# Kernel tuning notes

Hardware: AMD Instinct MI355X
Metric: run time of the kernel (lower is better)

The kernel has to match this reference:

```python
import jax, jax.numpy as jnp
import numpy as np

DIM = 512; NHEAD = 8; DHEAD = 64; INNER = NHEAD * DHEAD
CTX = 1024; NOCT = int(np.ceil(np.log2(CTX))) + 1  # 11
B = 8; SEQ = 256; MEM = 768


def positional_encoding(ctx, num_oct):
    # matches Attention.positional_encoding on coords=arange(ctx).view(ctx,1),
    # start_octave = 1 - num_oct
    coords = jnp.arange(ctx, dtype=jnp.float32)[:, None, None]        # (ctx,1,1)
    octaves = jnp.arange(1 - num_oct, 1, dtype=jnp.float32)           # (num_oct,)
    mult = (2.0 ** octaves) * np.pi
    scaled = (coords * mult).reshape(ctx, num_oct)                    # (ctx, num_oct)
    return jnp.concatenate([jnp.sin(scaled), jnp.cos(scaled)], axis=-1)  # (ctx, 2*num_oct)


def get_shifts(mem, seq, ctx):
    coords = jnp.arange(mem + seq - 1, -1, -1) - (seq - 1)            # (mem+seq,)
    shifts = coords[None, :] + jnp.arange(seq)[:, None]               # (seq, mem+seq)
    oob = (shifts < 0) | (shifts > ctx - 1)
    bias = jnp.where(oob, -jnp.inf, 0.0).astype(jnp.float32)
    return jnp.clip(shifts, 0, ctx - 1), bias


def setup_inputs() -> dict:
    key = jax.random.key(0)
    ks = jax.random.split(key, 8)
    s = 0.02
    return {
        "x": jax.random.normal(ks[0], (B, SEQ, DIM), jnp.float32),
        "memory": jax.random.normal(ks[1], (B, MEM, DIM), jnp.float32),
        "W_qkv": jax.random.normal(ks[2], (DIM, 3 * INNER), jnp.float32) * s,
        "W_rel": jax.random.normal(ks[3], (2 * NOCT, INNER), jnp.float32) * s,
        "W_out": jax.random.normal(ks[4], (INNER, DIM), jnp.float32) * s,
        "b_out": jnp.zeros((DIM,), jnp.float32),
        "u_emb": jax.random.normal(ks[5], (DHEAD,), jnp.float32),
        "v_emb": jax.random.normal(ks[6], (DHEAD,), jnp.float32),
    }


def reference(x, memory, W_qkv, W_rel, W_out, b_out, u_emb, v_emb):
    b, seq, _ = x.shape
    mem = memory.shape[1]
    total = mem + seq
    scale = DHEAD ** -0.5

    shifts, bias = get_shifts(mem, seq, CTX)                          # (seq,total) each
    R = positional_encoding(CTX, NOCT)                                # (CTX, 2*NOCT)
    kr = (R @ W_rel)[shifts].reshape(seq, total, NHEAD, DHEAD)        # n m h d

    qkv = jnp.concatenate([memory, x], axis=1) @ W_qkv                # (b,total,3*INNER)
    q, k, v = jnp.split(qkv, 3, axis=-1)

    def heads(t):
        return t.reshape(b, total, NHEAD, DHEAD).transpose(0, 2, 1, 3)  # b h m d

    q = heads(q)[:, :, mem:]                                          # b h n d (queries only over x)
    k = heads(k)
    v = heads(v)

    term_a = jnp.einsum('bhnd,bhmd->bhnm', q, k)
    term_b = jnp.einsum('bhnd,nmhd->bhnm', q, kr)
    term_c = jnp.einsum('d,bhmd->bhm', u_emb, k)[:, :, None, :]        # broadcast over n
    term_d = jnp.einsum('d,nmhd->hnm', v_emb, kr)[None]                # broadcast over b

    dots = (term_a + term_b + term_c + term_d) * scale + bias          # banded -inf mask
    attn = jax.nn.softmax(dots, axis=-1)                               # dropout p=0 -> identity
    out = jnp.einsum('bhnm,bhmd->bnhd', attn, v).reshape(b, seq, INNER)
    return out @ W_out + b_out
```

## Files before the change

### kernel.cpp

```cpp
#include <hip/hip_runtime.h>
#include <hip/hip_bf16.h>
#include <math.h>

typedef unsigned short u16;
typedef unsigned int u32;
typedef __attribute__((ext_vector_type(8))) short short8;
typedef __attribute__((ext_vector_type(4))) float floatx4;

constexpr int kB     = 8;
constexpr int kSEQ   = 256;
constexpr int kMEM   = 768;
constexpr int kTOTAL = 1024;

__device__ __forceinline__ float bf2f(u16 u) {
  return __uint_as_float(((u32)u) << 16);
}
__device__ __forceinline__ u16 f2bf(float f) {
  __hip_bfloat16 h = __float2bfloat16(f);
  return *reinterpret_cast<u16*>(&h);
}
__device__ __forceinline__ void gload_lds16(const u16* g, u16* l) {
  __builtin_amdgcn_global_load_lds(
      (__attribute__((address_space(1))) const unsigned int*)g,
      (__attribute__((address_space(3))) unsigned int*)l, 16, 0, 0);
}

__device__ __forceinline__ void wtconv_body(
    const float* __restrict__ W, u16* __restrict__ Wt, int K, int N,
    int n0, int k0, int tid, float (*tile)[65])
{
  int r = tid >> 4, c4 = (tid & 15) * 4;
#pragma unroll
  for (int v = 0; v < 4; v++) {
    float4 w4 = *(const float4*)(W + (size_t)(k0 + v * 16 + r) * N + n0 + c4);
    tile[v * 16 + r][c4 + 0] = w4.x;
    tile[v * 16 + r][c4 + 1] = w4.y;
    tile[v * 16 + r][c4 + 2] = w4.z;
    tile[v * 16 + r][c4 + 3] = w4.w;
  }
  __syncthreads();
#pragma unroll
  for (int v = 0; v < 4; v++) {
    int rn = v * 16 + r;
    ushort4 o;
    o.x = f2bf(tile[c4 + 0][rn]);
    o.y = f2bf(tile[c4 + 1][rn]);
    o.z = f2bf(tile[c4 + 2][rn]);
    o.w = f2bf(tile[c4 + 3][rn]);
    *(ushort4*)(Wt + (size_t)(n0 + rn) * K + k0 + c4) = o;
  }
}

__global__ __launch_bounds__(256) void prep_kernel(
    const float* __restrict__ x, const float* __restrict__ memf,
    const float* __restrict__ W_qkv, const float* __restrict__ W_out,
    const float* __restrict__ W_rel, const float* __restrict__ v_emb,
    const float* __restrict__ u_emb,
    u16* __restrict__ Xb, u16* __restrict__ WqkvT, u16* __restrict__ WoutT,
    u16* __restrict__ Rrel_bf, float* __restrict__ vR)
{
  __shared__ float tile[64][65];
  __shared__ float pe[22];
  __shared__ float prod[512];
  int bid = blockIdx.x;
  int t = threadIdx.x;
  if (bid < 1024) {
    int s = bid;
    if (t < 22) {
      int o = (t < 11) ? t : (t - 11);
      float mult = ldexpf(3.14159265358979323846f, o - 10);
      float ang = (float)s * mult;
      pe[t] = (t < 11) ? sinf(ang) : cosf(ang);
    }
    __syncthreads();
#pragma unroll
    for (int c = 0; c < 2; c++) {
      int j = t + c * 256;
      float acc = 0.f;
#pragma unroll
      for (int o = 0; o < 22; ++o) acc += pe[o] * W_rel[o * 512 + j];
      u16 rbf = f2bf(acc);
      Rrel_bf[(size_t)s * 512 + j] = rbf;
      prod[j] = acc * v_emb[j & 63] - bf2f(rbf) * u_emb[j & 63];
    }
    __syncthreads();
    if (t < 8) {
      float a = 0.f;
#pragma unroll 8
      for (int d = 0; d < 64; d++) a += prod[t * 64 + d];
      vR[t * 1024 + s] = a * 0.125f;
    }
  } else if (bid < 3072) {
    int idx = (bid - 1024) * 256 + t;
    int row = idx >> 6, c8 = idx & 63;
    int b = row >> 10, pos = row & 1023;
    const float* src = (pos < kMEM)
        ? memf + (size_t)(b * kMEM + pos) * 512
        : x    + (size_t)(b * kSEQ + pos - kMEM) * 512;
    const float4* s4 = (const float4*)(src + c8 * 8);
    float4 a = s4[0], bb = s4[1];
    u16 tmp[8] = {f2bf(a.x),  f2bf(a.y),  f2bf(a.z),  f2bf(a.w),
                  f2bf(bb.x), f2bf(bb.y), f2bf(bb.z), f2bf(bb.w)};
    *(uint4*)(Xb + (size_t)row * 512 + c8 * 8) = *(uint4*)tmp;
  } else if (bid < 3264) {
    int r = bid - 3072;
    wtconv_body(W_qkv, WqkvT, 512, 1536, (r % 24) * 64, (r / 24) * 64, t, tile);
  } else {
    int r = bid - 3264;
    wtconv_body(W_out, WoutT, 512, 512, (r % 8) * 64, (r / 8) * 64, t, tile);
  }
}

__global__ __launch_bounds__(256) void gemm_bf16(
    const u16* __restrict__ A, const u16* __restrict__ Bt,
    int lda, int ldb, int ksteps,
    u16* __restrict__ Cbf, int ldc, int qscale, const float* __restrict__ uq)
{
  __shared__ u16 As[128 * 64];
  __shared__ u16 Bs[128 * 64];
  int tid = threadIdx.x;
  int id = blockIdx.y * gridDim.x + blockIdx.x;
  int gy = gridDim.y;
  int bm = (id % gy) * 128, bn = (id / gy) * 128;
  if (qscale && bn < 512 && ((bm >> 7) & 7) < 6) return;
  int ln = tid & 15, quad = (tid >> 4) & 3, w = tid >> 6;
  int moff = (w >> 1) * 64, noff = (w & 1) * 64;
  int l7 = ln & 7;
  floatx4 acc[4][4];
#pragma unroll
  for (int mi = 0; mi < 4; mi++)
#pragma unroll
    for (int ni = 0; ni < 4; ni++) acc[mi][ni] = (floatx4){0.f, 0.f, 0.f, 0.f};

  int srow[4], sgch[4];
#pragma unroll
  for (int v = 0; v < 4; v++) {
    int f = v * 256 + tid;
    srow[v] = f >> 3;
    sgch[v] = (f & 7) ^ ((f >> 3) & 7);
  }

  for (int ks = 0; ks < ksteps; ks++) {
    int k0 = ks * 64;
#pragma unroll
    for (int v = 0; v < 4; v++) {
      gload_lds16(A + (size_t)(bm + srow[v]) * lda + k0 + sgch[v] * 8,
                  &As[(v * 256 + tid) * 8]);
      gload_lds16(Bt + (size_t)(bn + srow[v]) * ldb + k0 + sgch[v] * 8,
                  &Bs[(v * 256 + tid) * 8]);
    }
    __syncthreads();
#pragma unroll
    for (int kb = 0; kb < 2; kb++) {
      short8 af[4], bfr[4];
#pragma unroll
      for (int mi = 0; mi < 4; mi++) {
        int row = moff + mi * 16 + ln;
        af[mi] = *(const short8*)&As[row * 64 + (((quad + 4 * kb) ^ l7) << 3)];
      }
#pragma unroll
      for (int ni = 0; ni < 4; ni++) {
        int row = noff + ni * 16 + ln;
        bfr[ni] = *(const short8*)&Bs[row * 64 + (((quad + 4 * kb) ^ l7) << 3)];
      }
#pragma unroll
      for (int mi = 0; mi < 4; mi++)
#pragma unroll
        for (int ni = 0; ni < 4; ni++)
          acc[mi][ni] = __builtin_amdgcn_mfma_f32_16x16x32_bf16(
              af[mi], bfr[ni], acc[mi][ni], 0, 0, 0);
    }
    __syncthreads();
  }

  int r0 = bm + moff + quad * 4;
#pragma unroll
  for (int ni = 0; ni < 4; ni++) {
    int col = bn + noff + ni * 16 + ln;
    bool isq = qscale && col < 512;
    float scale = isq ? 0.125f : 1.f;
    float uadd = isq ? uq[col & 63] : 0.f;
#pragma unroll
    for (int mi = 0; mi < 4; mi++) {
#pragma unroll
      for (int r = 0; r < 4; r++) {
        int row = r0 + mi * 16 + r;
        Cbf[(size_t)row * ldc + col] = f2bf((acc[mi][ni][r] + uadd) * scale);
      }
    }
  }
}

__global__ __launch_bounds__(256) void gemm_bf16_64(
    const u16* __restrict__ A, const u16* __restrict__ Bt,
    int lda, int ldb, int ksteps,
    float* __restrict__ Cf, int ldc, const float* __restrict__ bias)
{
  __shared__ u16 As[64 * 64];
  __shared__ u16 Bs[64 * 64];
  int tid = threadIdx.x;
  int id = blockIdx.y * gridDim.x + blockIdx.x;
  int gy = gridDim.y;
  int bm = (id % gy) * 64, bn = (id / gy) * 64;
  int ln = tid & 15, quad = (tid >> 4) & 3, w = tid >> 6;
  int moff = (w >> 1) * 32, noff = (w & 1) * 32;
  int l7 = ln & 7;
  floatx4 acc[2][2];
#pragma unroll
  for (int mi = 0; mi < 2; mi++)
#pragma unroll
    for (int ni = 0; ni < 2; ni++) acc[mi][ni] = (floatx4){0.f, 0.f, 0.f, 0.f};

  int srow[2], sgch[2];
#pragma unroll
  for (int v = 0; v < 2; v++) {
    int f = v * 256 + tid;
    srow[v] = f >> 3;
    sgch[v] = (f & 7) ^ ((f >> 3) & 7);
  }

  for (int ks = 0; ks < ksteps; ks++) {
    int k0 = ks * 64;
#pragma unroll
    for (int v = 0; v < 2; v++) {
      gload_lds16(A + (size_t)(bm + srow[v]) * lda + k0 + sgch[v] * 8,
                  &As[(v * 256 + tid) * 8]);
      gload_lds16(Bt + (size_t)(bn + srow[v]) * ldb + k0 + sgch[v] * 8,
                  &Bs[(v * 256 + tid) * 8]);
    }
    __syncthreads();
#pragma unroll
    for (int kb = 0; kb < 2; kb++) {
      short8 af[2], bfr[2];
#pragma unroll
      for (int mi = 0; mi < 2; mi++) {
        int row = moff + mi * 16 + ln;
        af[mi] = *(const short8*)&As[row * 64 + (((quad + 4 * kb) ^ l7) << 3)];
      }
#pragma unroll
      for (int ni = 0; ni < 2; ni++) {
        int row = noff + ni * 16 + ln;
        bfr[ni] = *(const short8*)&Bs[row * 64 + (((quad + 4 * kb) ^ l7) << 3)];
      }
#pragma unroll
      for (int mi = 0; mi < 2; mi++)
#pragma unroll
        for (int ni = 0; ni < 2; ni++)
          acc[mi][ni] = __builtin_amdgcn_mfma_f32_16x16x32_bf16(
              af[mi], bfr[ni], acc[mi][ni], 0, 0, 0);
    }
    __syncthreads();
  }

  int r0 = bm + moff + quad * 4;
#pragma unroll
  for (int ni = 0; ni < 2; ni++) {
    int col = bn + noff + ni * 16 + ln;
    float cv = bias[col];
#pragma unroll
    for (int mi = 0; mi < 2; mi++) {
#pragma unroll
      for (int r = 0; r < 4; r++) {
        int row = r0 + mi * 16 + r;
        Cf[(size_t)row * ldc + col] = acc[mi][ni][r] + cv;
      }
    }
  }
}

__global__ __launch_bounds__(256) void attn_mfma(
    const u16* __restrict__ qkv_bf, const u16* __restrict__ Rrel_bf,
    const float* __restrict__ vR,
    u16* __restrict__ Opart, float* __restrict__ lbuf)
{
  constexpr int LD = 72;
  __shared__ u16 Vt[4][64 * LD];
  __shared__ u16 Ps[64 * LD];

  int h = blockIdx.x;
  int nt = blockIdx.y >> 1, p = blockIdx.y & 1;
  int b = blockIdx.z;
  int n0 = nt * 64, bh = b * 8 + h;
  int tid = threadIdx.x;
  int w = tid >> 6, lane = tid & 63;
  int l15 = lane & 15, quad = lane >> 4, q8 = quad * 8;

  int sr0 = tid >> 3, sc8 = tid & 7;
  int sr1 = (256 + tid) >> 3;
  int vg0 = ((sr0 >> 3) ^ sc8) * 8 + (sr0 & 7);
  int vg1 = ((sr1 >> 3) ^ sc8) * 8 + (sr1 & 7);

  const u16* kpart = qkv_bf + (size_t)(b * kTOTAL) * 1536 + 512 + h * 64;
  const float* vRh = vR + h * 1024;
  int s_base_w = kMEM + n0 + 16 * w;

  const u16* qrow = qkv_bf + (size_t)(b * kTOTAL + kMEM + n0 + 16 * w + l15) * 1536 + h * 64;
  short8 qf0 = *(const short8*)(qrow + q8);
  short8 qf1 = *(const short8*)(qrow + 32 + q8);

  int bidx[4];
#pragma unroll
  for (int r = 0; r < 4; r++) {
    int il = 4 * quad + r;
    bidx[r] = ((quad << 4) | ((il + 15 - l15) & 15)) << 2;
  }

  auto load_V = [&](int mtu, int mtv, uint4 (&vr)[4]) {
    const u16* va = kpart + (size_t)mtu * 64 * 1536 + 512;
    const u16* vb = kpart + (size_t)mtv * 64 * 1536 + 512;
    vr[0] = *(const uint4*)(va + (size_t)sr0 * 1536 + sc8 * 8);
    vr[1] = *(const uint4*)(va + (size_t)sr1 * 1536 + sc8 * 8);
    vr[2] = *(const uint4*)(vb + (size_t)sr0 * 1536 + sc8 * 8);
    vr[3] = *(const uint4*)(vb + (size_t)sr1 * 1536 + sc8 * 8);
  };
  auto write_V = [&](uint4 (&vr)[4], u16* bu, u16* bv) {
    const u16* c0 = (const u16*)&vr[0];
    const u16* c1 = (const u16*)&vr[1];
    const u16* c2 = (const u16*)&vr[2];
    const u16* c3 = (const u16*)&vr[3];
#pragma unroll
    for (int i = 0; i < 8; i++) {
      bu[(sc8 * 8 + i) * LD + vg0] = c0[i];
      bu[(sc8 * 8 + i) * LD + vg1] = c1[i];
      bv[(sc8 * 8 + i) * LD + vg0] = c2[i];
      bv[(sc8 * 8 + i) * LD + vg1] = c3[i];
    }
  };
  auto load_K = [&](int mt, short8 (&k0)[4], short8 (&k1)[4]) {
#pragma unroll
    for (int ni = 0; ni < 4; ni++) {
      const u16* kr = kpart + (size_t)(mt * 64 + 16 * ni + l15) * 1536;
      k0[ni] = *(const short8*)(kr + q8);
      k1[ni] = *(const short8*)(kr + 32 + q8);
    }
  };
  auto load_R = [&](int sb, short8 (&r0)[5], short8 (&r1)[5], float (&vc)[5]) {
#pragma unroll
    for (int ct = 0; ct < 5; ct++) {
      int s = sb - 63 + 16 * ct + l15;
      s = min(max(s, 0), 1023);
      const u16* rr = Rrel_bf + (size_t)s * 512 + h * 64;
      r0[ct] = *(const short8*)(rr + q8);
      r1[ct] = *(const short8*)(rr + 32 + q8);
      vc[ct] = vRh[s];
    }
  };

  floatx4 o_acc[4];
  float l_i[4];
#pragma unroll
  for (int r = 0; r < 4; r++) l_i[r] = 0.f;
#pragma unroll
  for (int nd = 0; nd < 4; nd++) o_acc[nd] = (floatx4){0.f, 0.f, 0.f, 0.f};

  auto do_T = [&](short8 (&rb0)[5], short8 (&rb1)[5], float (&vRc)[5],
                  float (&tf)[5][4]) {
#pragma unroll
    for (int ct = 0; ct < 5; ct++) {
      floatx4 t = (floatx4){0.f, 0.f, 0.f, 0.f};
      t = __builtin_amdgcn_mfma_f32_16x16x32_bf16(qf0, rb0[ct], t, 0, 0, 0);
      t = __builtin_amdgcn_mfma_f32_16x16x32_bf16(qf1, rb1[ct], t, 0, 0, 0);
#pragma unroll
      for (int r = 0; r < 4; r++) tf[ct][r] = t[r] + vRc[ct];
    }
  };
  auto do_tsh = [&](float (&tf)[5][4], float (&tsh)[4][4]) {
#pragma unroll
    for (int ni = 0; ni < 4; ni++) {
#pragma unroll
      for (int r = 0; r < 4; r++) {
        int il = 4 * quad + r;
        float tv = (l15 < il) ? tf[4 - ni][r] : tf[3 - ni][r];
        tsh[ni][r] = __int_as_float(
            __builtin_amdgcn_ds_bpermute(bidx[r], __float_as_int(tv)));
      }
    }
  };
  auto do_QK = [&](short8 (&kb0)[4], short8 (&kb1)[4], floatx4 (&sa)[4]) {
#pragma unroll
    for (int ni = 0; ni < 4; ni++) {
      floatx4 s4 = (floatx4){0.f, 0.f, 0.f, 0.f};
      s4 = __builtin_amdgcn_mfma_f32_16x16x32_bf16(qf0, kb0[ni], s4, 0, 0, 0);
      s4 = __builtin_amdgcn_mfma_f32_16x16x32_bf16(qf1, kb1[ni], s4, 0, 0, 0);
      sa[ni] = s4;
    }
  };
  auto do_logits = [&](floatx4 (&sa)[4], float (&tsh)[4][4], int sb) {
#pragma unroll
    for (int ni = 0; ni < 4; ni++) {
#pragma unroll
      for (int r = 0; r < 4; r++) {
        int il = 4 * quad + r;
        float val = sa[ni][r] + tsh[ni][r];
        if ((16 * ni + l15) > (sb + il)) val = -1e30f;
        float e = __expf(val);
        l_i[r] += e;
        int prow = 16 * w + il;
        Ps[prow * LD + (l15 & 7) + (((2 * ni + (l15 >> 3)) ^ (prow >> 3)) << 3)] =
            f2bf(e);
      }
    }
  };
  auto do_PV = [&](const u16* VtX) {
    int rowq = 16 * w + l15, rr3q = rowq >> 3;
    short8 pa0 = *(const short8*)&Ps[rowq * LD + ((quad ^ rr3q) << 3)];
    short8 pa1 = *(const short8*)&Ps[rowq * LD + (((quad + 4) ^ rr3q) << 3)];
#pragma unroll
    for (int nd = 0; nd < 4; nd++) {
      int rowv = 16 * nd + l15, rr3v = rowv >> 3;
      short8 vb0 = *(const short8*)&VtX[rowv * LD + ((quad ^ rr3v) << 3)];
      short8 vb1 = *(const short8*)&VtX[rowv * LD + (((quad + 4) ^ rr3v) << 3)];
      o_acc[nd] = __builtin_amdgcn_mfma_f32_16x16x32_bf16(pa0, vb0, o_acc[nd], 0, 0, 0);
      o_acc[nd] = __builtin_amdgcn_mfma_f32_16x16x32_bf16(pa1, vb1, o_acc[nd], 0, 0, 0);
    }
  };

  uint4 vsl[2][4];
  short8 rbP0[2][5], rbP1[2][5];
  float vRcP[2][5];
  load_V(p, p + 2, vsl[0]);
  write_V(vsl[0], Vt[0], Vt[1]);
  load_V(p + 4, p + 6, vsl[1]);
  load_R(s_base_w - 64 * p, rbP0[0], rbP1[0], vRcP[0]);
  __syncthreads();

#pragma unroll
  for (int g = 0; g < 4; g++) {
    int mtU = p + 4 * g, mtV = p + 4 * g + 2;
    int sbU = s_base_w - 64 * mtU, sbV = s_base_w - 64 * mtV;

    if (g < 3) write_V(vsl[(g + 1) & 1], Vt[2 * ((g + 1) & 1)], Vt[2 * ((g + 1) & 1) + 1]);
    if (g < 2) load_V(p + 4 * g + 8, p + 4 * g + 10, vsl[g & 1]);

    short8 kbU0[4], kbU1[4];
    load_K(mtU, kbU0, kbU1);

    float tfU[5][4], tshU[4][4];
    do_T(rbP0[g & 1], rbP1[g & 1], vRcP[g & 1], tfU);
    do_tsh(tfU, tshU);

    short8 rbV0[5], rbV1[5];
    float vRcV[5];
    load_R(sbV, rbV0, rbV1, vRcV);

    floatx4 saU[4];
    do_QK(kbU0, kbU1, saU);
    do_logits(saU, tshU, sbU);

    short8 kbV0[4], kbV1[4];
    load_K(mtV, kbV0, kbV1);
    if (g < 3)
      load_R(s_base_w - 64 * (p + 4 * (g + 1)),
             rbP0[(g + 1) & 1], rbP1[(g + 1) & 1], vRcP[(g + 1) & 1]);

    float tfV[5][4], tshV[4][4];
    do_T(rbV0, rbV1, vRcV, tfV);
    do_tsh(tfV, tshV);

    do_PV(Vt[2 * (g & 1)]);

    floatx4 saV[4];
    do_QK(kbV0, kbV1, saV);
    do_logits(saV, tshV, sbV);
    do_PV(Vt[2 * (g & 1) + 1]);

    if (g < 3) __syncthreads();
  }

  int pbase = (p * 64 + bh) * 256;
#pragma unroll
  for (int r = 0; r < 4; r++) {
    float l = l_i[r];
#pragma unroll
    for (int off = 1; off < 16; off <<= 1)
      l += __shfl_xor(l, off, 64);
    int n = n0 + 16 * w + 4 * quad + r;
    u16* orow = Opart + ((size_t)(pbase + n) << 6) + l15;
#pragma unroll
    for (int nd = 0; nd < 4; nd++)
      orow[16 * nd] = f2bf(o_acc[nd][r]);
    if (l15 == 0) lbuf[pbase + n] = l;
  }
}

__global__ __launch_bounds__(256) void attn_combine(
    const u16* __restrict__ Opart, const float* __restrict__ lbuf,
    u16* __restrict__ aout_bf)
{
  int idx = blockIdx.x * 256 + threadIdx.x;
  int bh = idx >> 12, n = (idx >> 4) & 255, d4 = idx & 15;
  int rowi = bh * 256 + n;
  float den = 0.f;
  float num[4] = {0.f, 0.f, 0.f, 0.f};
#pragma unroll
  for (int p = 0; p < 2; p++) {
    den += lbuf[(p << 14) + rowi];
    uint2 raw = *(const uint2*)(Opart + (((size_t)(p << 14) + rowi) << 6) + d4 * 4);
    const u16* us = (const u16*)&raw;
#pragma unroll
    for (int j = 0; j < 4; j++) num[j] += bf2f(us[j]);
  }
  float inv = 1.f / den;
  int b = bh >> 3, h = bh & 7;
  ushort4 o;
  o.x = f2bf(num[0] * inv);
  o.y = f2bf(num[1] * inv);
  o.z = f2bf(num[2] * inv);
  o.w = f2bf(num[3] * inv);
  *(ushort4*)(aout_bf + (size_t)(b * kSEQ + n) * 512 + h * 64 + d4 * 4) = o;
}

extern "C" void kernel_launch(void* const* d_in, const int* in_sizes, int n_in,
                              void* d_out, int out_size, void* d_ws, size_t ws_size,
                              hipStream_t stream) {
  (void)in_sizes; (void)n_in; (void)out_size; (void)ws_size;
  const float* x      = (const float*)d_in[0];
  const float* memory = (const float*)d_in[1];
  const float* W_qkv  = (const float*)d_in[2];
  const float* W_rel  = (const float*)d_in[3];
  const float* W_out  = (const float*)d_in[4];
  const float* b_out  = (const float*)d_in[5];
  const float* u_emb  = (const float*)d_in[6];
  const float* v_emb  = (const float*)d_in[7];
  float* out = (float*)d_out;

  char* ws = (char*)d_ws;
  u16*   qkv_bf  = (u16*)ws;                         ws += (size_t)12582912 * 2;
  u16*   Xcat_bf = (u16*)ws;                         ws += (size_t)4194304 * 2;
  u16*   aout_bf = (u16*)ws;                         ws += (size_t)1048576 * 2;
  u16*   Opart   = (u16*)ws;                         ws += (size_t)2097152 * 2;
  float* lbuf    = (float*)ws;                       ws += (size_t)32768 * 4;
  u16*   WqkvT   = (u16*)ws;                         ws += (size_t)786432 * 2;
  u16*   WoutT   = (u16*)ws;                         ws += (size_t)262144 * 2;
  u16*   Rrel_bf = (u16*)ws;                         ws += (size_t)524288 * 2;
  float* vR      = (float*)ws;                       ws += (size_t)8192 * 4;

  prep_kernel<<<3328, 256, 0, stream>>>(
      x, memory, W_qkv, W_out, W_rel, v_emb, u_emb,
      Xcat_bf, WqkvT, WoutT, Rrel_bf, vR);

  gemm_bf16<<<dim3(12, 64), 256, 0, stream>>>(
      Xcat_bf, WqkvT, 512, 512, 8, qkv_bf, 1536, 1, u_emb);

  attn_mfma<<<dim3(8, 8, 8), 256, 0, stream>>>(
      qkv_bf, Rrel_bf, vR, Opart, lbuf);

  attn_combine<<<1024, 256, 0, stream>>>(Opart, lbuf, aout_bf);

  gemm_bf16_64<<<dim3(8, 32), 256, 0, stream>>>(
      aout_bf, WoutT, 512, 512, 8, out, 512, b_out);
}
```

Measured before the change: 155.6 us.

## Split attention key range four ways instead of two across blocks

The attention kernel now splits each (b,h,query-tile) over four key partitions instead of two. The grid doubles to 1024 blocks and each block handles 4 key tiles instead of 8, with the V double-buffer pipeline reduced to a single 2-tile stage plus one refill. The combine kernel sums four partials and the partial buffers double in size. This is meant to fill more compute units on the MI355X, at the cost of more partial-output traffic, more redundant Q loads, and less intra-block pipelining.

```diff
diff --git a/kernel.cpp b/kernel.cpp
--- a/kernel.cpp
+++ b/kernel.cpp
@@ -274,11 +274,11 @@
     u16* __restrict__ Opart, float* __restrict__ lbuf)
 {
   constexpr int LD = 72;
-  __shared__ u16 Vt[4][64 * LD];
+  __shared__ u16 Vt[2][64 * LD];
   __shared__ u16 Ps[64 * LD];
 
   int h = blockIdx.x;
-  int nt = blockIdx.y >> 1, p = blockIdx.y & 1;
+  int nt = blockIdx.y >> 2, p = blockIdx.y & 3;
   int b = blockIdx.z;
   int n0 = nt * 64, bh = b * 8 + h;
   int tid = threadIdx.x;
@@ -415,28 +415,30 @@
     }
   };
 
-  uint4 vsl[2][4];
-  short8 rbP0[2][5], rbP1[2][5];
-  float vRcP[2][5];
-  load_V(p, p + 2, vsl[0]);
-  write_V(vsl[0], Vt[0], Vt[1]);
-  load_V(p + 4, p + 6, vsl[1]);
-  load_R(s_base_w - 64 * p, rbP0[0], rbP1[0], vRcP[0]);
+  short8 rbU0[5], rbU1[5];
+  float vRcU[5];
+  uint4 vsl[4];
+  {
+    uint4 v0[4];
+    load_V(p, p + 4, v0);
+    write_V(v0, Vt[0], Vt[1]);
+  }
+  load_V(p + 8, p + 12, vsl);
+  load_R(s_base_w - 64 * p, rbU0, rbU1, vRcU);
   __syncthreads();
 
 #pragma unroll
-  for (int g = 0; g < 4; g++) {
-    int mtU = p + 4 * g, mtV = p + 4 * g + 2;
+  for (int g = 0; g < 2; g++) {
+    int mtU = p + 8 * g, mtV = mtU + 4;
     int sbU = s_base_w - 64 * mtU, sbV = s_base_w - 64 * mtV;
 
-    if (g < 3) write_V(vsl[(g + 1) & 1], Vt[2 * ((g + 1) & 1)], Vt[2 * ((g + 1) & 1) + 1]);
-    if (g < 2) load_V(p + 4 * g + 8, p + 4 * g + 10, vsl[g & 1]);
+    if (g == 1) write_V(vsl, Vt[0], Vt[1]);
 
     short8 kbU0[4], kbU1[4];
     load_K(mtU, kbU0, kbU1);
 
     float tfU[5][4], tshU[4][4];
-    do_T(rbP0[g & 1], rbP1[g & 1], vRcP[g & 1], tfU);
+    do_T(rbU0, rbU1, vRcU, tfU);
     do_tsh(tfU, tshU);
 
     short8 rbV0[5], rbV1[5];
@@ -449,22 +451,22 @@
 
     short8 kbV0[4], kbV1[4];
     load_K(mtV, kbV0, kbV1);
-    if (g < 3)
-      load_R(s_base_w - 64 * (p + 4 * (g + 1)),
-             rbP0[(g + 1) & 1], rbP1[(g + 1) & 1], vRcP[(g + 1) & 1]);
+    if (g == 0)
+      load_R(s_base_w - 64 * (p + 8), rbU0, rbU1, vRcU);
 
     float tfV[5][4], tshV[4][4];
     do_T(rbV0, rbV1, vRcV, tfV);
     do_tsh(tfV, tshV);
 
-    do_PV(Vt[2 * (g & 1)]);
+    if (g == 1) __syncthreads();
+    do_PV(Vt[0]);
 
     floatx4 saV[4];
     do_QK(kbV0, kbV1, saV);
     do_logits(saV, tshV, sbV);
-    do_PV(Vt[2 * (g & 1) + 1]);
-
-    if (g < 3) __syncthreads();
+    do_PV(Vt[1]);
+
+    if (g == 0) __syncthreads();
   }
 
   int pbase = (p * 64 + bh) * 256;
@@ -493,7 +495,7 @@
   float den = 0.f;
   float num[4] = {0.f, 0.f, 0.f, 0.f};
 #pragma unroll
-  for (int p = 0; p < 2; p++) {
+  for (int p = 0; p < 4; p++) {
     den += lbuf[(p << 14) + rowi];
     uint2 raw = *(const uint2*)(Opart + (((size_t)(p << 14) + rowi) << 6) + d4 * 4);
     const u16* us = (const u16*)&raw;
@@ -528,8 +530,8 @@
   u16*   qkv_bf  = (u16*)ws;                         ws += (size_t)12582912 * 2;
   u16*   Xcat_bf = (u16*)ws;                         ws += (size_t)4194304 * 2;
   u16*   aout_bf = (u16*)ws;                         ws += (size_t)1048576 * 2;
-  u16*   Opart   = (u16*)ws;                         ws += (size_t)2097152 * 2;
-  float* lbuf    = (float*)ws;                       ws += (size_t)32768 * 4;
+  u16*   Opart   = (u16*)ws;                         ws += (size_t)4194304 * 2;
+  float* lbuf    = (float*)ws;                       ws += (size_t)65536 * 4;
   u16*   WqkvT   = (u16*)ws;                         ws += (size_t)786432 * 2;
   u16*   WoutT   = (u16*)ws;                         ws += (size_t)262144 * 2;
   u16*   Rrel_bf = (u16*)ws;                         ws += (size_t)524288 * 2;
@@ -542,7 +544,7 @@
   gemm_bf16<<<dim3(12, 64), 256, 0, stream>>>(
       Xcat_bf, WqkvT, 512, 512, 8, qkv_bf, 1536, 1, u_emb);
 
-  attn_mfma<<<dim3(8, 8, 8), 256, 0, stream>>>(
+  attn_mfma<<<dim3(8, 16, 8), 256, 0, stream>>>(
       qkv_bf, Rrel_bf, vR, Opart, lbuf);
 
   attn_combine<<<1024, 256, 0, stream>>>(Opart, lbuf, aout_bf);
```

New measurement: 150.3 us. -3.4%, faster.
